# Performance work log

Measured on AMD Instinct MI355X. Metric: run time of the kernel, lower is better.

## Reference

```python
import jax, jax.numpy as jnp
import numpy as np

# Dimensions (see shape_source): k=4 -> hk=cobj_size=2
K_LEVEL = 4
HK = K_LEVEL // 2            # conv kernel/stride, == cobj_size
BS = 16                      # MBS*ncobj groups
NUM_TOP = 512
BAG = 50                     # bag size B (orig_fea.shape[1])
D = 512                      # feature dim
H = 512                      # relation-unit hidden dim


def setup_inputs() -> dict:
    key = jax.random.key(0)
    ks = jax.random.split(key, 7)
    orig_fea = jax.random.normal(ks[0], (BS * 2 * HK, BAG, D), jnp.float32)
    ind0 = jax.random.randint(ks[1], (BS, NUM_TOP, HK), 0, BAG, jnp.int32)
    ind1 = jax.random.randint(ks[2], (BS, NUM_TOP, HK), 0, BAG, jnp.int32)
    W0 = jax.random.normal(ks[3], (D, H), jnp.float32) * 0.05
    W1 = jax.random.normal(ks[4], (D, H), jnp.float32) * 0.05
    b = jax.random.normal(ks[5], (H,), jnp.float32) * 0.05
    v = jax.random.normal(ks[6], (H,), jnp.float32) * 0.05
    return {"orig_fea": orig_fea, "ind0": ind0, "ind1": ind1,
            "W0": W0, "W1": W1, "b": b, "v": v}


def reference(orig_fea, ind0, ind1, W0, W1, b, v):
    bs = ind0.shape[0]
    bag = orig_fea.shape[1]
    cobj = ind0.shape[-1]                 # == k//2 == conv kernel hk
    d = orig_fea.shape[-1]

    # create_ids: offset by bag * position so ids index into the flattened half
    offs = (bag * jnp.arange(cobj)).astype(ind0.dtype)
    ids0 = (ind0 + offs).reshape(bs, -1)  # [bs, S], S = num_top*cobj
    ids1 = (ind1 + offs).reshape(bs, -1)

    # rsolo_fea: [bs, 2, X, D] with X = bag*cobj
    fea = orig_fea.reshape(bs, 2, -1, d)

    # relation unit over ALL X*X candidate pairs (dedupe+gather-back in the
    # original is pure memoization; compute-then-gather is the same math)
    h0 = jnp.einsum('bxd,dh->bxh', fea[:, 0], W0)   # [bs, X, H]
    h1 = jnp.einsum('byd,dh->byh', fea[:, 1], W1)   # [bs, X, H]
    hid = jax.nn.relu(h0[:, :, None, :] + h1[:, None, :, :] + b)  # [bs, X, X, H]
    full = jnp.einsum('bxyh,h->bxy', hid, v)        # [bs, X, X]

    # gather rows by ids0, cols by ids1 (per group)
    scores = jax.vmap(lambda f, i0, i1: f[i0][:, i1])(full, ids0, ids1)  # [bs, S, S]

    # Conv2D(1, kernel=hk, stride=hk, ones kernel, zero bias) == block sum-pool
    S = scores.shape[1]
    hk = cobj
    pooled = scores.reshape(bs, S // hk, hk, S // hk, hk).sum(axis=(2, 4))  # [bs, nt, nt]
    out_scores = pooled.reshape(bs, -1, 1)          # [bs, nt*nt, 1]

    nt0, nt1 = ind0.shape[1], ind1.shape[1]
    gi, gj = jnp.meshgrid(jnp.arange(nt0, dtype=jnp.int32),
                          jnp.arange(nt1, dtype=jnp.int32), indexing='ij')
    pairs = jnp.broadcast_to(jnp.stack([gi, gj], axis=-1)[None],
                             (bs, nt0, nt1, 2)).reshape(bs, nt0 * nt1, 2)
    return out_scores, pairs
```

## Files before the change

kernel.cpp:

```cpp
#include <hip/hip_runtime.h>

#define XDIM  100
#define DDIM  512
#define HDIM  512
#define NT    512
#define WS_WT2   0
#define WS_FEA16 1048576
#define WS_V16   4325376
#define WS_H16   4326400
#define WS_FP    7603200
#define WS_FPS   12723200

typedef _Float16 h16x8 __attribute__((ext_vector_type(8)));
typedef _Float16 h2    __attribute__((ext_vector_type(2)));
typedef float floatx4  __attribute__((ext_vector_type(4)));
typedef float floatx2  __attribute__((ext_vector_type(2)));

union H8U { h16x8 v; h2 p[4]; unsigned u[4]; };

__global__ void __launch_bounds__(256) prep_k(const float* __restrict__ W0,
                                              const float* __restrict__ W1,
                                              const float* __restrict__ fea,
                                              const float* __restrict__ v,
                                              _Float16* __restrict__ Wt2,
                                              _Float16* __restrict__ fea16,
                                              _Float16* __restrict__ v16) {
    int blk = blockIdx.x;
    int t = threadIdx.x;
    if (blk < 2048) {
        int o  = blk * 256 + t;
        int w  = o >> 18;
        int kb = (o >> 14) & 15;
        int c  = (o >> 5) & 511;
        int qj = o & 31;
        int d  = kb * 32 + qj;
        const float* W = w ? W1 : W0;
        Wt2[o] = (_Float16)W[d * 512 + c];
    } else if (blk < 3648) {
        int tid = (blk - 2048) * 256 + t;
        float4 x = *(const float4*)(fea + (size_t)tid * 4);
        _Float16 r[4] = {(_Float16)x.x, (_Float16)x.y, (_Float16)x.z, (_Float16)x.w};
        *(uint2*)(fea16 + (size_t)tid * 4) = *(const uint2*)r;
    } else {
        v16[t * 2]     = (_Float16)v[t * 2];
        v16[t * 2 + 1] = (_Float16)v[t * 2 + 1];
    }
}

__global__ void __launch_bounds__(256) gemm_k(const _Float16* __restrict__ fea16,
                                              const _Float16* __restrict__ Wt2,
                                              const float* __restrict__ bias,
                                              _Float16* __restrict__ h16) {
    int bx   = blockIdx.x;
    int hb   = bx / 14;
    int rem  = bx % 14;
    int rt   = rem >> 1;
    int chal = rem & 1;
    int w    = threadIdx.x >> 6;
    int lane = threadIdx.x & 63;
    int n0   = (chal * 4 + w) * 64;
    int m0   = rt * 16;
    int s    = hb & 1;
    int l15  = lane & 15;
    int q    = lane >> 4;
    int m    = min(m0 + l15, XDIM - 1);

    const _Float16* ap = fea16 + (size_t)hb * (XDIM * DDIM) + (size_t)m * DDIM + q * 8;
    const _Float16* bp = Wt2 + (size_t)s * 262144 + (size_t)(n0 + l15) * 32 + q * 8;

    floatx4 acc0 = {0.f, 0.f, 0.f, 0.f};
    floatx4 acc1 = acc0, acc2 = acc0, acc3 = acc0;

    for (int kb = 0; kb < 16; ++kb) {
        h16x8 a = *(const h16x8*)(ap + kb * 32);
        const _Float16* bkb = bp + kb * 16384;
        h16x8 b0 = *(const h16x8*)(bkb);
        h16x8 b1 = *(const h16x8*)(bkb + 512);
        h16x8 b2 = *(const h16x8*)(bkb + 1024);
        h16x8 b3 = *(const h16x8*)(bkb + 1536);
        acc0 = __builtin_amdgcn_mfma_f32_16x16x32_f16(a, b0, acc0, 0, 0, 0);
        acc1 = __builtin_amdgcn_mfma_f32_16x16x32_f16(a, b1, acc1, 0, 0, 0);
        acc2 = __builtin_amdgcn_mfma_f32_16x16x32_f16(a, b2, acc2, 0, 0, 0);
        acc3 = __builtin_amdgcn_mfma_f32_16x16x32_f16(a, b3, acc3, 0, 0, 0);
    }

    _Float16* hob = h16 + (size_t)hb * (XDIM * HDIM);
    #pragma unroll
    for (int j = 0; j < 4; ++j) {
        floatx4 a = (j == 0) ? acc0 : (j == 1) ? acc1 : (j == 2) ? acc2 : acc3;
        int col = n0 + 16 * j + l15;
        float bi = s ? bias[col] : 0.f;
        #pragma unroll
        for (int r = 0; r < 4; ++r) {
            int mr = m0 + q * 4 + r;
            if (mr < XDIM) hob[(size_t)mr * HDIM + col] = (_Float16)(a[r] + bi);
        }
    }
}

__global__ void __launch_bounds__(256) full_k(const _Float16* __restrict__ h16,
                                              const _Float16* __restrict__ v16,
                                              float* __restrict__ fp,
                                              float* __restrict__ pout) {
    int bx  = blockIdx.x;
    int ks  = bx >> 6;
    int rem = bx & 63;
    int b   = rem >> 2;
    int xt  = (rem >> 1) & 1;
    int yt  = rem & 1;
    int x0  = xt * 36;
    int y0  = yt * 36;
    int kc  = ks * 64;

    __shared__ _Float16 sh0[64][72];
    __shared__ unsigned sh1p[32][64];
    __shared__ unsigned sv[32];

    int t = threadIdx.x;
    int r = t & 63, kseg = t >> 6;

    const _Float16* g0 = h16 + ((size_t)(b * 2) * XDIM + x0 + r) * HDIM + kc + kseg * 16;
    *(h16x8*)&sh0[r][kseg * 16]     = *(const h16x8*)g0;
    *(h16x8*)&sh0[r][kseg * 16 + 8] = *(const h16x8*)(g0 + 8);

    const _Float16* g1 = h16 + ((size_t)(b * 2 + 1) * XDIM + y0 + r) * HDIM + kc + kseg * 16;
    H8U u0, u1;
    u0.v = *(const h16x8*)g1;
    u1.v = *(const h16x8*)(g1 + 8);
    #pragma unroll
    for (int pp = 0; pp < 4; ++pp) {
        sh1p[kseg * 8 + pp][r]     = u0.u[pp];
        sh1p[kseg * 8 + 4 + pp][r] = u1.u[pp];
    }
    if (t < 32) sv[t] = *(const unsigned*)(v16 + kc + t * 2);
    __syncthreads();

    {
        size_t pbase = (size_t)bx * 8192;
        #pragma unroll 4
        for (int i = 0; i < 32; ++i) {
            unsigned idx = (unsigned)(pbase + i * 256 + t);
            floatx2 pr;
            pr.x = (float)((idx >> 9) & 511);
            pr.y = (float)(idx & 511);
            __builtin_nontemporal_store(pr, (floatx2*)(pout + (size_t)idx * 2));
        }
    }

    int ty = t >> 4, tx = t & 15;
    float acc[4][4] = {};
    h2 hz; hz[0] = (_Float16)0; hz[1] = (_Float16)0;

    for (int kk = 0; kk < 8; ++kk) {
        H8U a[4];
        #pragma unroll
        for (int i = 0; i < 4; ++i)
            a[i].v = *(const h16x8*)&sh0[ty * 4 + i][kk * 8];
        uint4 bq[4];
        #pragma unroll
        for (int p = 0; p < 4; ++p)
            bq[p] = *(const uint4*)&sh1p[kk * 4 + p][tx * 4];
        uint4 vq = *(const uint4*)&sv[kk * 4];
        const unsigned* vqa = (const unsigned*)&vq;

        #pragma unroll
        for (int p = 0; p < 4; ++p) {
            h2 vp = __builtin_bit_cast(h2, vqa[p]);
            const unsigned* bqa = (const unsigned*)&bq[p];
            #pragma unroll
            for (int i = 0; i < 4; ++i) {
                h2 av = a[i].p[p];
                #pragma unroll
                for (int j = 0; j < 4; ++j) {
                    h2 s = av + __builtin_bit_cast(h2, bqa[j]);
                    s = __builtin_elementwise_max(s, hz);
#if __has_builtin(__builtin_amdgcn_fdot2)
                    acc[i][j] = __builtin_amdgcn_fdot2(s, vp, acc[i][j], false);
#else
                    acc[i][j] += (float)s[0] * (float)vp[0] + (float)s[1] * (float)vp[1];
#endif
                }
            }
        }
    }

    float* fpb = fp + (size_t)(ks * 16 + b) * (XDIM * XDIM);
    #pragma unroll
    for (int i = 0; i < 4; ++i) {
        floatx4 o;
        o.x = acc[i][0]; o.y = acc[i][1]; o.z = acc[i][2]; o.w = acc[i][3];
        *(floatx4*)&fpb[(size_t)(x0 + ty * 4 + i) * XDIM + y0 + tx * 4] = o;
    }
}

__global__ void __launch_bounds__(256) fold_k(const float* __restrict__ fp,
                                              float* __restrict__ fps) {
    int vi = blockIdx.x * 256 + threadIdx.x;
    if (vi >= 40000) return;
    const floatx4* f4 = (const floatx4*)fp;
    floatx4 s = f4[vi];
    #pragma unroll
    for (int ks = 1; ks < 8; ++ks) {
        floatx4 u = f4[(size_t)ks * 40000 + vi];
        s.x += u.x; s.y += u.y; s.z += u.z; s.w += u.w;
    }
    *(floatx4*)(fps + (size_t)vi * 4) = s;
}

__global__ void __launch_bounds__(256) score_k(const float* __restrict__ fps,
                                               const int* __restrict__ ind0,
                                               const int* __restrict__ ind1,
                                               float* __restrict__ out) {
    int bx  = blockIdx.x;
    int b   = bx >> 5;
    int rem = bx & 31;
    int it  = rem >> 1;
    int jh  = rem & 1;
    int i0  = it * 32;

    __shared__ float rowsum[32][100];
    __shared__ int a0s[32], a1s[32];
    __shared__ int c0s[256], c1s[256];

    int t = threadIdx.x;
    if (t < 32) {
        int2 ii = *(const int2*)(ind0 + ((size_t)b * NT + i0 + t) * 2);
        a0s[t] = ii.x;
        a1s[t] = ii.y + 50;
    }
    {
        int2 jj = *(const int2*)(ind1 + ((size_t)b * NT + jh * 256 + t) * 2);
        c0s[t] = jj.x;
        c1s[t] = jj.y + 50;
    }
    __syncthreads();

    const float* fb = fps + (size_t)b * (XDIM * XDIM);
    for (int idx = t; idx < 1024; idx += 256) {
        int il = idx >> 5, yq = idx & 31;
        if (yq < 25) {
            floatx4 u = *(const floatx4*)(fb + a0s[il] * XDIM + yq * 4);
            floatx4 w = *(const floatx4*)(fb + a1s[il] * XDIM + yq * 4);
            floatx4 s;
            s.x = u.x + w.x; s.y = u.y + w.y;
            s.z = u.z + w.z; s.w = u.w + w.w;
            *(floatx4*)&rowsum[il][yq * 4] = s;
        }
    }
    __syncthreads();

    float* sout = out + (size_t)b * (NT * NT) + (size_t)i0 * NT + jh * 256;
    for (int o = t; o < 8192; o += 256) {
        int il = o >> 8, jl = o & 255;
        float val = rowsum[il][c0s[jl]] + rowsum[il][c1s[jl]];
        __builtin_nontemporal_store(val, &sout[(size_t)il * NT + jl]);
    }
}

extern "C" void kernel_launch(void* const* d_in, const int* in_sizes, int n_in,
                              void* d_out, int out_size, void* d_ws, size_t ws_size,
                              hipStream_t stream) {
    const float* fea  = (const float*)d_in[0];
    const int*   ind0 = (const int*)d_in[1];
    const int*   ind1 = (const int*)d_in[2];
    const float* W0   = (const float*)d_in[3];
    const float* W1   = (const float*)d_in[4];
    const float* bias = (const float*)d_in[5];
    const float* v    = (const float*)d_in[6];
    float* out = (float*)d_out;
    char*  ws  = (char*)d_ws;

    _Float16* Wt2   = (_Float16*)(ws + WS_WT2);
    _Float16* fea16 = (_Float16*)(ws + WS_FEA16);
    _Float16* v16   = (_Float16*)(ws + WS_V16);
    _Float16* h16   = (_Float16*)(ws + WS_H16);
    float*    fp    = (float*)(ws + WS_FP);
    float*    fps   = (float*)(ws + WS_FPS);
    float*    pout  = (float*)(out + (size_t)16 * NT * NT);

    hipLaunchKernelGGL(prep_k,  dim3(3649), dim3(256), 0, stream, W0, W1, fea, v, Wt2, fea16, v16);
    hipLaunchKernelGGL(gemm_k,  dim3(448),  dim3(256), 0, stream, fea16, Wt2, bias, h16);
    hipLaunchKernelGGL(full_k,  dim3(512),  dim3(256), 0, stream, h16, v16, fp, pout);
    hipLaunchKernelGGL(fold_k,  dim3(157),  dim3(256), 0, stream, fp, fps);
    hipLaunchKernelGGL(score_k, dim3(512),  dim3(256), 0, stream, fps, ind0, ind1, out);
}
```

Before: 118.6 us.

## Replace split-K partial buffer and fold kernel with atomic accumulation

The relation-score kernel now adds its split-K partial sums straight into the final score buffer with atomic adds. This removes the intermediate partial buffer and the separate fold kernel, and prep_k zeroes the destination instead. The pair-index output writes are divided between gemm_k and full_k, and gemm_k is re-tiled to 512 blocks covering rows in overlapping 36-row halves. This saves one launch and a round trip of the partial buffer, at the cost of atomic contention and non-deterministic float summation order.

```diff
diff --git a/kernel.cpp b/kernel.cpp
--- a/kernel.cpp
+++ b/kernel.cpp
@@ -8,8 +8,7 @@
 #define WS_FEA16 1048576
 #define WS_V16   4325376
 #define WS_H16   4326400
-#define WS_FP    7603200
-#define WS_FPS   12723200
+#define WS_FPS   7603200
 
 typedef _Float16 h16x8 __attribute__((ext_vector_type(8)));
 typedef _Float16 h2    __attribute__((ext_vector_type(2)));
@@ -24,7 +23,8 @@
                                               const float* __restrict__ v,
                                               _Float16* __restrict__ Wt2,
                                               _Float16* __restrict__ fea16,
-                                              _Float16* __restrict__ v16) {
+                                              _Float16* __restrict__ v16,
+                                              float* __restrict__ fps) {
     int blk = blockIdx.x;
     int t = threadIdx.x;
     if (blk < 2048) {
@@ -41,31 +41,48 @@
         float4 x = *(const float4*)(fea + (size_t)tid * 4);
         _Float16 r[4] = {(_Float16)x.x, (_Float16)x.y, (_Float16)x.z, (_Float16)x.w};
         *(uint2*)(fea16 + (size_t)tid * 4) = *(const uint2*)r;
-    } else {
+    } else if (blk == 3648) {
         v16[t * 2]     = (_Float16)v[t * 2];
         v16[t * 2 + 1] = (_Float16)v[t * 2 + 1];
+    } else {
+        int vi = (blk - 3649) * 256 + t;
+        if (vi < 40000) {
+            floatx4 z = {0.f, 0.f, 0.f, 0.f};
+            *(floatx4*)(fps + (size_t)vi * 4) = z;
+        }
     }
 }
 
 __global__ void __launch_bounds__(256) gemm_k(const _Float16* __restrict__ fea16,
                                               const _Float16* __restrict__ Wt2,
                                               const float* __restrict__ bias,
-                                              _Float16* __restrict__ h16) {
+                                              _Float16* __restrict__ h16,
+                                              float* __restrict__ pout) {
     int bx   = blockIdx.x;
-    int hb   = bx / 14;
-    int rem  = bx % 14;
-    int rt   = rem >> 1;
-    int chal = rem & 1;
+    int hb   = bx >> 4;
+    int mt   = (bx >> 3) & 1;
+    int no   = bx & 7;
     int w    = threadIdx.x >> 6;
     int lane = threadIdx.x & 63;
-    int n0   = (chal * 4 + w) * 64;
-    int m0   = rt * 16;
+    int n0   = no * 64;
+    int m0   = mt * 36 + w * 16;
     int s    = hb & 1;
     int l15  = lane & 15;
     int q    = lane >> 4;
-    int m    = min(m0 + l15, XDIM - 1);
-
-    const _Float16* ap = fea16 + (size_t)hb * (XDIM * DDIM) + (size_t)m * DDIM + q * 8;
+
+    {
+        size_t pbase = (size_t)bx * 4096;
+        #pragma unroll 4
+        for (int i = 0; i < 16; ++i) {
+            unsigned idx = (unsigned)(pbase + i * 256 + threadIdx.x);
+            floatx2 pr;
+            pr.x = (float)((idx >> 9) & 511);
+            pr.y = (float)(idx & 511);
+            __builtin_nontemporal_store(pr, (floatx2*)(pout + (size_t)idx * 2));
+        }
+    }
+
+    const _Float16* ap = fea16 + (size_t)hb * (XDIM * DDIM) + (size_t)(m0 + l15) * DDIM + q * 8;
     const _Float16* bp = Wt2 + (size_t)s * 262144 + (size_t)(n0 + l15) * 32 + q * 8;
 
     floatx4 acc0 = {0.f, 0.f, 0.f, 0.f};
@@ -93,14 +110,14 @@
         #pragma unroll
         for (int r = 0; r < 4; ++r) {
             int mr = m0 + q * 4 + r;
-            if (mr < XDIM) hob[(size_t)mr * HDIM + col] = (_Float16)(a[r] + bi);
+            hob[(size_t)mr * HDIM + col] = (_Float16)(a[r] + bi);
         }
     }
 }
 
 __global__ void __launch_bounds__(256) full_k(const _Float16* __restrict__ h16,
                                               const _Float16* __restrict__ v16,
-                                              float* __restrict__ fp,
+                                              float* __restrict__ fps,
                                               float* __restrict__ pout) {
     int bx  = blockIdx.x;
     int ks  = bx >> 6;
@@ -136,9 +153,9 @@
     __syncthreads();
 
     {
-        size_t pbase = (size_t)bx * 8192;
+        size_t pbase = 2097152 + (size_t)bx * 4096;
         #pragma unroll 4
-        for (int i = 0; i < 32; ++i) {
+        for (int i = 0; i < 16; ++i) {
             unsigned idx = (unsigned)(pbase + i * 256 + t);
             floatx2 pr;
             pr.x = (float)((idx >> 9) & 511);
@@ -184,27 +201,16 @@
         }
     }
 
-    float* fpb = fp + (size_t)(ks * 16 + b) * (XDIM * XDIM);
-    #pragma unroll
-    for (int i = 0; i < 4; ++i) {
-        floatx4 o;
-        o.x = acc[i][0]; o.y = acc[i][1]; o.z = acc[i][2]; o.w = acc[i][3];
-        *(floatx4*)&fpb[(size_t)(x0 + ty * 4 + i) * XDIM + y0 + tx * 4] = o;
-    }
-}
-
-__global__ void __launch_bounds__(256) fold_k(const float* __restrict__ fp,
-                                              float* __restrict__ fps) {
-    int vi = blockIdx.x * 256 + threadIdx.x;
-    if (vi >= 40000) return;
-    const floatx4* f4 = (const floatx4*)fp;
-    floatx4 s = f4[vi];
-    #pragma unroll
-    for (int ks = 1; ks < 8; ++ks) {
-        floatx4 u = f4[(size_t)ks * 40000 + vi];
-        s.x += u.x; s.y += u.y; s.z += u.z; s.w += u.w;
-    }
-    *(floatx4*)(fps + (size_t)vi * 4) = s;
+    if ((xt == 0 || ty >= 7) && (yt == 0 || tx >= 7)) {
+        float* fpb = fps + (size_t)b * (XDIM * XDIM);
+        #pragma unroll
+        for (int i = 0; i < 4; ++i) {
+            #pragma unroll
+            for (int j = 0; j < 4; ++j)
+                unsafeAtomicAdd(&fpb[(size_t)(x0 + ty * 4 + i) * XDIM + y0 + tx * 4 + j],
+                                acc[i][j]);
+        }
+    }
 }
 
 __global__ void __launch_bounds__(256) score_k(const float* __restrict__ fps,
@@ -274,13 +280,11 @@
     _Float16* fea16 = (_Float16*)(ws + WS_FEA16);
     _Float16* v16   = (_Float16*)(ws + WS_V16);
     _Float16* h16   = (_Float16*)(ws + WS_H16);
-    float*    fp    = (float*)(ws + WS_FP);
     float*    fps   = (float*)(ws + WS_FPS);
     float*    pout  = (float*)(out + (size_t)16 * NT * NT);
 
-    hipLaunchKernelGGL(prep_k,  dim3(3649), dim3(256), 0, stream, W0, W1, fea, v, Wt2, fea16, v16);
-    hipLaunchKernelGGL(gemm_k,  dim3(448),  dim3(256), 0, stream, fea16, Wt2, bias, h16);
-    hipLaunchKernelGGL(full_k,  dim3(512),  dim3(256), 0, stream, h16, v16, fp, pout);
-    hipLaunchKernelGGL(fold_k,  dim3(157),  dim3(256), 0, stream, fp, fps);
+    hipLaunchKernelGGL(prep_k,  dim3(3806), dim3(256), 0, stream, W0, W1, fea, v, Wt2, fea16, v16, fps);
+    hipLaunchKernelGGL(gemm_k,  dim3(512),  dim3(256), 0, stream, fea16, Wt2, bias, h16, pout);
+    hipLaunchKernelGGL(full_k,  dim3(512),  dim3(256), 0, stream, h16, v16, fps, pout);
     hipLaunchKernelGGL(score_k, dim3(512),  dim3(256), 0, stream, fps, ind0, ind1, out);
 }
```

After: 130.8 us. 1.1x slower.

## Fuse five kernels into one cooperative persistent kernel with grid syncs

Applied to the files above, without the earlier changes.

Replaces the five separate launches (prep, gemm, full, fold, score) with one cooperative kernel of 512 blocks that runs every stage in sequence, separated by grid.sync(). The GEMM stage is re-tiled from 448 to 512 blocks, with row tiles at offsets 0 and 36 so every block has work. The aim is to remove per-launch overhead and the idle gaps between kernels. In exchange, each grid-wide barrier has a cost, and the shared-memory footprint is the union of all stages, which may limit occupancy. Cooperative launch also requires all 512 blocks to be resident at once.

```diff
diff --git a/kernel.cpp b/kernel.cpp
--- a/kernel.cpp
+++ b/kernel.cpp
@@ -1,4 +1,7 @@
 #include <hip/hip_runtime.h>
+#include <hip/hip_cooperative_groups.h>
+
+namespace cg = cooperative_groups;
 
 #define XDIM  100
 #define DDIM  512
@@ -18,17 +21,32 @@
 
 union H8U { h16x8 v; h2 p[4]; unsigned u[4]; };
 
-__global__ void __launch_bounds__(256) prep_k(const float* __restrict__ W0,
-                                              const float* __restrict__ W1,
-                                              const float* __restrict__ fea,
-                                              const float* __restrict__ v,
-                                              _Float16* __restrict__ Wt2,
-                                              _Float16* __restrict__ fea16,
-                                              _Float16* __restrict__ v16) {
-    int blk = blockIdx.x;
-    int t = threadIdx.x;
-    if (blk < 2048) {
-        int o  = blk * 256 + t;
+__global__ void __launch_bounds__(256, 2) fused_k(
+    const float* __restrict__ fea,  const int* __restrict__ ind0,
+    const int* __restrict__ ind1,   const float* __restrict__ W0,
+    const float* __restrict__ W1,   const float* __restrict__ bias,
+    const float* __restrict__ v,
+    _Float16* __restrict__ Wt2,  _Float16* __restrict__ fea16,
+    _Float16* __restrict__ v16,  _Float16* __restrict__ h16,
+    float* __restrict__ fp,      float* __restrict__ fps,
+    float* __restrict__ out,     float* __restrict__ pout)
+{
+    cg::grid_group grid = cg::this_grid();
+
+    __shared__ _Float16 sh0[64][72];
+    __shared__ unsigned sh1p[32][64];
+    __shared__ unsigned sv[32];
+    __shared__ float rowsum[32][100];
+    __shared__ int a0s[32], a1s[32];
+    __shared__ int c0s[256], c1s[256];
+
+    const int bx = blockIdx.x;
+    const int t  = threadIdx.x;
+    const int gtid = bx * 256 + t;
+
+    #pragma unroll
+    for (int i = 0; i < 4; ++i) {
+        int o  = gtid + i * 131072;
         int w  = o >> 18;
         int kb = (o >> 14) & 15;
         int c  = (o >> 5) & 511;
@@ -36,224 +54,202 @@
         int d  = kb * 32 + qj;
         const float* W = w ? W1 : W0;
         Wt2[o] = (_Float16)W[d * 512 + c];
-    } else if (blk < 3648) {
-        int tid = (blk - 2048) * 256 + t;
-        float4 x = *(const float4*)(fea + (size_t)tid * 4);
+    }
+    for (int i = gtid; i < 409600; i += 131072) {
+        float4 x = *(const float4*)(fea + (size_t)i * 4);
         _Float16 r[4] = {(_Float16)x.x, (_Float16)x.y, (_Float16)x.z, (_Float16)x.w};
-        *(uint2*)(fea16 + (size_t)tid * 4) = *(const uint2*)r;
-    } else {
-        v16[t * 2]     = (_Float16)v[t * 2];
-        v16[t * 2 + 1] = (_Float16)v[t * 2 + 1];
-    }
-}
-
-__global__ void __launch_bounds__(256) gemm_k(const _Float16* __restrict__ fea16,
-                                              const _Float16* __restrict__ Wt2,
-                                              const float* __restrict__ bias,
-                                              _Float16* __restrict__ h16) {
-    int bx   = blockIdx.x;
-    int hb   = bx / 14;
-    int rem  = bx % 14;
-    int rt   = rem >> 1;
-    int chal = rem & 1;
-    int w    = threadIdx.x >> 6;
-    int lane = threadIdx.x & 63;
-    int n0   = (chal * 4 + w) * 64;
-    int m0   = rt * 16;
-    int s    = hb & 1;
-    int l15  = lane & 15;
-    int q    = lane >> 4;
-    int m    = min(m0 + l15, XDIM - 1);
-
-    const _Float16* ap = fea16 + (size_t)hb * (XDIM * DDIM) + (size_t)m * DDIM + q * 8;
-    const _Float16* bp = Wt2 + (size_t)s * 262144 + (size_t)(n0 + l15) * 32 + q * 8;
-
-    floatx4 acc0 = {0.f, 0.f, 0.f, 0.f};
-    floatx4 acc1 = acc0, acc2 = acc0, acc3 = acc0;
-
-    for (int kb = 0; kb < 16; ++kb) {
-        h16x8 a = *(const h16x8*)(ap + kb * 32);
-        const _Float16* bkb = bp + kb * 16384;
-        h16x8 b0 = *(const h16x8*)(bkb);
-        h16x8 b1 = *(const h16x8*)(bkb + 512);
-        h16x8 b2 = *(const h16x8*)(bkb + 1024);
-        h16x8 b3 = *(const h16x8*)(bkb + 1536);
-        acc0 = __builtin_amdgcn_mfma_f32_16x16x32_f16(a, b0, acc0, 0, 0, 0);
-        acc1 = __builtin_amdgcn_mfma_f32_16x16x32_f16(a, b1, acc1, 0, 0, 0);
-        acc2 = __builtin_amdgcn_mfma_f32_16x16x32_f16(a, b2, acc2, 0, 0, 0);
-        acc3 = __builtin_amdgcn_mfma_f32_16x16x32_f16(a, b3, acc3, 0, 0, 0);
-    }
-
-    _Float16* hob = h16 + (size_t)hb * (XDIM * HDIM);
-    #pragma unroll
-    for (int j = 0; j < 4; ++j) {
-        floatx4 a = (j == 0) ? acc0 : (j == 1) ? acc1 : (j == 2) ? acc2 : acc3;
-        int col = n0 + 16 * j + l15;
-        float bi = s ? bias[col] : 0.f;
-        #pragma unroll
-        for (int r = 0; r < 4; ++r) {
-            int mr = m0 + q * 4 + r;
-            if (mr < XDIM) hob[(size_t)mr * HDIM + col] = (_Float16)(a[r] + bi);
-        }
-    }
-}
-
-__global__ void __launch_bounds__(256) full_k(const _Float16* __restrict__ h16,
-                                              const _Float16* __restrict__ v16,
-                                              float* __restrict__ fp,
-                                              float* __restrict__ pout) {
-    int bx  = blockIdx.x;
-    int ks  = bx >> 6;
-    int rem = bx & 63;
-    int b   = rem >> 2;
-    int xt  = (rem >> 1) & 1;
-    int yt  = rem & 1;
-    int x0  = xt * 36;
-    int y0  = yt * 36;
-    int kc  = ks * 64;
-
-    __shared__ _Float16 sh0[64][72];
-    __shared__ unsigned sh1p[32][64];
-    __shared__ unsigned sv[32];
-
-    int t = threadIdx.x;
-    int r = t & 63, kseg = t >> 6;
-
-    const _Float16* g0 = h16 + ((size_t)(b * 2) * XDIM + x0 + r) * HDIM + kc + kseg * 16;
-    *(h16x8*)&sh0[r][kseg * 16]     = *(const h16x8*)g0;
-    *(h16x8*)&sh0[r][kseg * 16 + 8] = *(const h16x8*)(g0 + 8);
-
-    const _Float16* g1 = h16 + ((size_t)(b * 2 + 1) * XDIM + y0 + r) * HDIM + kc + kseg * 16;
-    H8U u0, u1;
-    u0.v = *(const h16x8*)g1;
-    u1.v = *(const h16x8*)(g1 + 8);
-    #pragma unroll
-    for (int pp = 0; pp < 4; ++pp) {
-        sh1p[kseg * 8 + pp][r]     = u0.u[pp];
-        sh1p[kseg * 8 + 4 + pp][r] = u1.u[pp];
-    }
-    if (t < 32) sv[t] = *(const unsigned*)(v16 + kc + t * 2);
-    __syncthreads();
+        *(uint2*)(fea16 + (size_t)i * 4) = *(const uint2*)r;
+    }
+    if (gtid < 256) {
+        v16[gtid * 2]     = (_Float16)v[gtid * 2];
+        v16[gtid * 2 + 1] = (_Float16)v[gtid * 2 + 1];
+    }
+    grid.sync();
 
     {
-        size_t pbase = (size_t)bx * 8192;
-        #pragma unroll 4
-        for (int i = 0; i < 32; ++i) {
-            unsigned idx = (unsigned)(pbase + i * 256 + t);
-            floatx2 pr;
-            pr.x = (float)((idx >> 9) & 511);
-            pr.y = (float)(idx & 511);
-            __builtin_nontemporal_store(pr, (floatx2*)(pout + (size_t)idx * 2));
-        }
-    }
-
-    int ty = t >> 4, tx = t & 15;
-    float acc[4][4] = {};
-    h2 hz; hz[0] = (_Float16)0; hz[1] = (_Float16)0;
-
-    for (int kk = 0; kk < 8; ++kk) {
-        H8U a[4];
-        #pragma unroll
-        for (int i = 0; i < 4; ++i)
-            a[i].v = *(const h16x8*)&sh0[ty * 4 + i][kk * 8];
-        uint4 bq[4];
-        #pragma unroll
-        for (int p = 0; p < 4; ++p)
-            bq[p] = *(const uint4*)&sh1p[kk * 4 + p][tx * 4];
-        uint4 vq = *(const uint4*)&sv[kk * 4];
-        const unsigned* vqa = (const unsigned*)&vq;
-
-        #pragma unroll
-        for (int p = 0; p < 4; ++p) {
-            h2 vp = __builtin_bit_cast(h2, vqa[p]);
-            const unsigned* bqa = (const unsigned*)&bq[p];
-            #pragma unroll
-            for (int i = 0; i < 4; ++i) {
-                h2 av = a[i].p[p];
+        int hb   = bx >> 4;
+        int mt   = (bx >> 3) & 1;
+        int no   = bx & 7;
+        int w    = t >> 6;
+        int lane = t & 63;
+        int n0   = no * 64;
+        int m0   = mt * 36 + w * 16;
+        int s    = hb & 1;
+        int l15  = lane & 15;
+        int q    = lane >> 4;
+
+        const _Float16* ap = fea16 + (size_t)hb * (XDIM * DDIM) + (size_t)(m0 + l15) * DDIM + q * 8;
+        const _Float16* bp = Wt2 + (size_t)s * 262144 + (size_t)(n0 + l15) * 32 + q * 8;
+
+        floatx4 acc0 = {0.f, 0.f, 0.f, 0.f};
+        floatx4 acc1 = acc0, acc2 = acc0, acc3 = acc0;
+
+        for (int kb = 0; kb < 16; ++kb) {
+            h16x8 a = *(const h16x8*)(ap + kb * 32);
+            const _Float16* bkb = bp + kb * 16384;
+            h16x8 b0 = *(const h16x8*)(bkb);
+            h16x8 b1 = *(const h16x8*)(bkb + 512);
+            h16x8 b2 = *(const h16x8*)(bkb + 1024);
+            h16x8 b3 = *(const h16x8*)(bkb + 1536);
+            acc0 = __builtin_amdgcn_mfma_f32_16x16x32_f16(a, b0, acc0, 0, 0, 0);
+            acc1 = __builtin_amdgcn_mfma_f32_16x16x32_f16(a, b1, acc1, 0, 0, 0);
+            acc2 = __builtin_amdgcn_mfma_f32_16x16x32_f16(a, b2, acc2, 0, 0, 0);
+            acc3 = __builtin_amdgcn_mfma_f32_16x16x32_f16(a, b3, acc3, 0, 0, 0);
+        }
+
+        _Float16* hob = h16 + (size_t)hb * (XDIM * HDIM);
+        #pragma unroll
+        for (int j = 0; j < 4; ++j) {
+            floatx4 a = (j == 0) ? acc0 : (j == 1) ? acc1 : (j == 2) ? acc2 : acc3;
+            int col = n0 + 16 * j + l15;
+            float bi = s ? bias[col] : 0.f;
+            #pragma unroll
+            for (int r = 0; r < 4; ++r) {
+                int mr = m0 + q * 4 + r;
+                hob[(size_t)mr * HDIM + col] = (_Float16)(a[r] + bi);
+            }
+        }
+    }
+    grid.sync();
+
+    {
+        int ks  = bx >> 6;
+        int rem = bx & 63;
+        int b   = rem >> 2;
+        int xt  = (rem >> 1) & 1;
+        int yt  = rem & 1;
+        int x0  = xt * 36;
+        int y0  = yt * 36;
+        int kc  = ks * 64;
+
+        int r = t & 63, kseg = t >> 6;
+
+        const _Float16* g0 = h16 + ((size_t)(b * 2) * XDIM + x0 + r) * HDIM + kc + kseg * 16;
+        *(h16x8*)&sh0[r][kseg * 16]     = *(const h16x8*)g0;
+        *(h16x8*)&sh0[r][kseg * 16 + 8] = *(const h16x8*)(g0 + 8);
+
+        const _Float16* g1 = h16 + ((size_t)(b * 2 + 1) * XDIM + y0 + r) * HDIM + kc + kseg * 16;
+        H8U u0, u1;
+        u0.v = *(const h16x8*)g1;
+        u1.v = *(const h16x8*)(g1 + 8);
+        #pragma unroll
+        for (int pp = 0; pp < 4; ++pp) {
+            sh1p[kseg * 8 + pp][r]     = u0.u[pp];
+            sh1p[kseg * 8 + 4 + pp][r] = u1.u[pp];
+        }
+        if (t < 32) sv[t] = *(const unsigned*)(v16 + kc + t * 2);
+        __syncthreads();
+
+        {
+            size_t pbase = (size_t)bx * 8192;
+            #pragma unroll 4
+            for (int i = 0; i < 32; ++i) {
+                unsigned idx = (unsigned)(pbase + i * 256 + t);
+                floatx2 pr;
+                pr.x = (float)((idx >> 9) & 511);
+                pr.y = (float)(idx & 511);
+                __builtin_nontemporal_store(pr, (floatx2*)(pout + (size_t)idx * 2));
+            }
+        }
+
+        int ty = t >> 4, tx = t & 15;
+        float acc[4][4] = {};
+        h2 hz; hz[0] = (_Float16)0; hz[1] = (_Float16)0;
+
+        for (int kk = 0; kk < 8; ++kk) {
+            H8U a[4];
+            #pragma unroll
+            for (int i = 0; i < 4; ++i)
+                a[i].v = *(const h16x8*)&sh0[ty * 4 + i][kk * 8];
+            uint4 bq[4];
+            #pragma unroll
+            for (int p = 0; p < 4; ++p)
+                bq[p] = *(const uint4*)&sh1p[kk * 4 + p][tx * 4];
+            uint4 vq = *(const uint4*)&sv[kk * 4];
+            const unsigned* vqa = (const unsigned*)&vq;
+
+            #pragma unroll
+            for (int p = 0; p < 4; ++p) {
+                h2 vp = __builtin_bit_cast(h2, vqa[p]);
+                const unsigned* bqa = (const unsigned*)&bq[p];
                 #pragma unroll
-                for (int j = 0; j < 4; ++j) {
-                    h2 s = av + __builtin_bit_cast(h2, bqa[j]);
-                    s = __builtin_elementwise_max(s, hz);
+                for (int i = 0; i < 4; ++i) {
+                    h2 av = a[i].p[p];
+                    #pragma unroll
+                    for (int j = 0; j < 4; ++j) {
+                        h2 s = av + __builtin_bit_cast(h2, bqa[j]);
+                        s = __builtin_elementwise_max(s, hz);
 #if __has_builtin(__builtin_amdgcn_fdot2)
-                    acc[i][j] = __builtin_amdgcn_fdot2(s, vp, acc[i][j], false);
+                        acc[i][j] = __builtin_amdgcn_fdot2(s, vp, acc[i][j], false);
 #else
-                    acc[i][j] += (float)s[0] * (float)vp[0] + (float)s[1] * (float)vp[1];
+                        acc[i][j] += (float)s[0] * (float)vp[0] + (float)s[1] * (float)vp[1];
 #endif
+                    }
                 }
             }
         }
-    }
-
-    float* fpb = fp + (size_t)(ks * 16 + b) * (XDIM * XDIM);
-    #pragma unroll
-    for (int i = 0; i < 4; ++i) {
-        floatx4 o;
-        o.x = acc[i][0]; o.y = acc[i][1]; o.z = acc[i][2]; o.w = acc[i][3];
-        *(floatx4*)&fpb[(size_t)(x0 + ty * 4 + i) * XDIM + y0 + tx * 4] = o;
-    }
-}
-
-__global__ void __launch_bounds__(256) fold_k(const float* __restrict__ fp,
-                                              float* __restrict__ fps) {
-    int vi = blockIdx.x * 256 + threadIdx.x;
-    if (vi >= 40000) return;
-    const floatx4* f4 = (const floatx4*)fp;
-    floatx4 s = f4[vi];
-    #pragma unroll
-    for (int ks = 1; ks < 8; ++ks) {
-        floatx4 u = f4[(size_t)ks * 40000 + vi];
-        s.x += u.x; s.y += u.y; s.z += u.z; s.w += u.w;
-    }
-    *(floatx4*)(fps + (size_t)vi * 4) = s;
-}
-
-__global__ void __launch_bounds__(256) score_k(const float* __restrict__ fps,
-                                               const int* __restrict__ ind0,
-                                               const int* __restrict__ ind1,
-                                               float* __restrict__ out) {
-    int bx  = blockIdx.x;
-    int b   = bx >> 5;
-    int rem = bx & 31;
-    int it  = rem >> 1;
-    int jh  = rem & 1;
-    int i0  = it * 32;
-
-    __shared__ float rowsum[32][100];
-    __shared__ int a0s[32], a1s[32];
-    __shared__ int c0s[256], c1s[256];
-
-    int t = threadIdx.x;
-    if (t < 32) {
-        int2 ii = *(const int2*)(ind0 + ((size_t)b * NT + i0 + t) * 2);
-        a0s[t] = ii.x;
-        a1s[t] = ii.y + 50;
-    }
+
+        float* fpb = fp + (size_t)(ks * 16 + b) * (XDIM * XDIM);
+        #pragma unroll
+        for (int i = 0; i < 4; ++i) {
+            floatx4 o;
+            o.x = acc[i][0]; o.y = acc[i][1]; o.z = acc[i][2]; o.w = acc[i][3];
+            *(floatx4*)&fpb[(size_t)(x0 + ty * 4 + i) * XDIM + y0 + tx * 4] = o;
+        }
+    }
+    grid.sync();
+
+    if (gtid < 40000) {
+        const floatx4* f4 = (const floatx4*)fp;
+        floatx4 s = f4[gtid];
+        #pragma unroll
+        for (int ks = 1; ks < 8; ++ks) {
+            floatx4 u = f4[(size_t)ks * 40000 + gtid];
+            s.x += u.x; s.y += u.y; s.z += u.z; s.w += u.w;
+        }
+        *(floatx4*)(fps + (size_t)gtid * 4) = s;
+    }
+    grid.sync();
+
     {
-        int2 jj = *(const int2*)(ind1 + ((size_t)b * NT + jh * 256 + t) * 2);
-        c0s[t] = jj.x;
-        c1s[t] = jj.y + 50;
-    }
-    __syncthreads();
-
-    const float* fb = fps + (size_t)b * (XDIM * XDIM);
-    for (int idx = t; idx < 1024; idx += 256) {
-        int il = idx >> 5, yq = idx & 31;
-        if (yq < 25) {
-            floatx4 u = *(const floatx4*)(fb + a0s[il] * XDIM + yq * 4);
-            floatx4 w = *(const floatx4*)(fb + a1s[il] * XDIM + yq * 4);
-            floatx4 s;
-            s.x = u.x + w.x; s.y = u.y + w.y;
-            s.z = u.z + w.z; s.w = u.w + w.w;
-            *(floatx4*)&rowsum[il][yq * 4] = s;
-        }
-    }
-    __syncthreads();
-
-    float* sout = out + (size_t)b * (NT * NT) + (size_t)i0 * NT + jh * 256;
-    for (int o = t; o < 8192; o += 256) {
-        int il = o >> 8, jl = o & 255;
-        float val = rowsum[il][c0s[jl]] + rowsum[il][c1s[jl]];
-        __builtin_nontemporal_store(val, &sout[(size_t)il * NT + jl]);
+        int b   = bx >> 5;
+        int rem = bx & 31;
+        int it  = rem >> 1;
+        int jh  = rem & 1;
+        int i0  = it * 32;
+
+        if (t < 32) {
+            int2 ii = *(const int2*)(ind0 + ((size_t)b * NT + i0 + t) * 2);
+            a0s[t] = ii.x;
+            a1s[t] = ii.y + 50;
+        }
+        {
+            int2 jj = *(const int2*)(ind1 + ((size_t)b * NT + jh * 256 + t) * 2);
+            c0s[t] = jj.x;
+            c1s[t] = jj.y + 50;
+        }
+        __syncthreads();
+
+        const float* fb = fps + (size_t)b * (XDIM * XDIM);
+        for (int idx = t; idx < 1024; idx += 256) {
+            int il = idx >> 5, yq = idx & 31;
+            if (yq < 25) {
+                floatx4 u = *(const floatx4*)(fb + a0s[il] * XDIM + yq * 4);
+                floatx4 w = *(const floatx4*)(fb + a1s[il] * XDIM + yq * 4);
+                floatx4 s;
+                s.x = u.x + w.x; s.y = u.y + w.y;
+                s.z = u.z + w.z; s.w = u.w + w.w;
+                *(floatx4*)&rowsum[il][yq * 4] = s;
+            }
+        }
+        __syncthreads();
+
+        float* sout = out + (size_t)b * (NT * NT) + (size_t)i0 * NT + jh * 256;
+        for (int o = t; o < 8192; o += 256) {
+            int il = o >> 8, jl = o & 255;
+            float val = rowsum[il][c0s[jl]] + rowsum[il][c1s[jl]];
+            __builtin_nontemporal_store(val, &sout[(size_t)il * NT + jl]);
+        }
     }
 }
 
@@ -278,9 +274,9 @@
     float*    fps   = (float*)(ws + WS_FPS);
     float*    pout  = (float*)(out + (size_t)16 * NT * NT);
 
-    hipLaunchKernelGGL(prep_k,  dim3(3649), dim3(256), 0, stream, W0, W1, fea, v, Wt2, fea16, v16);
-    hipLaunchKernelGGL(gemm_k,  dim3(448),  dim3(256), 0, stream, fea16, Wt2, bias, h16);
-    hipLaunchKernelGGL(full_k,  dim3(512),  dim3(256), 0, stream, h16, v16, fp, pout);
-    hipLaunchKernelGGL(fold_k,  dim3(157),  dim3(256), 0, stream, fp, fps);
-    hipLaunchKernelGGL(score_k, dim3(512),  dim3(256), 0, stream, fps, ind0, ind1, out);
+    void* args[] = {(void*)&fea, (void*)&ind0, (void*)&ind1, (void*)&W0,
+                    (void*)&W1, (void*)&bias, (void*)&v,
+                    (void*)&Wt2, (void*)&fea16, (void*)&v16, (void*)&h16,
+                    (void*)&fp, (void*)&fps, (void*)&out, (void*)&pout};
+    hipLaunchCooperativeKernel((void*)fused_k, dim3(512), dim3(256), args, 0, stream);
 }
```

Result: slower. 374.1 us (+215.3%).
